# Performance work log

Hardware: AMD Instinct MI355X
Metric: run time of the kernel (lower is better)

## Reference

```python
import jax, jax.numpy as jnp
import numpy as np

N_QUBITS = 10
N_LAYERS = 4
BATCH = 16384
IN_FEAT = 256
HIDDEN = 128


def _ry(theta):
    # RY(theta) = [[cos(t/2), -sin(t/2)], [sin(t/2), cos(t/2)]]; theta: (B, n) -> (B, n, 2, 2)
    c = jnp.cos(theta / 2)
    s = jnp.sin(theta / 2)
    row0 = jnp.stack([c, -s], axis=-1)
    row1 = jnp.stack([s, c], axis=-1)
    return jnp.stack([row0, row1], axis=-2).astype(jnp.complex64)


def _rot(phi, theta, omega):
    # PennyLane Rot = RZ(omega) RY(theta) RZ(phi)
    c = jnp.cos(theta / 2)
    s = jnp.sin(theta / 2)
    ep = jnp.exp(-0.5j * (phi + omega))  # e^{-i(phi+omega)/2}
    em = jnp.exp(-0.5j * (phi - omega))  # e^{-i(phi-omega)/2}
    m00 = ep * c
    m01 = -jnp.conj(em) * s
    m10 = em * s
    m11 = jnp.conj(ep) * c
    return jnp.stack([jnp.stack([m00, m01]), jnp.stack([m10, m11])]).astype(jnp.complex64)


def _apply_1q(state, gate, w, n):
    # state: (B, 2**n); gate: (2,2) shared or (B,2,2) per-sample; wire w (wire 0 = MSB)
    B = state.shape[0]
    L, R = 2 ** w, 2 ** (n - w - 1)
    s = state.reshape(B, L, 2, R)
    if gate.ndim == 3:
        s = jnp.einsum('xab,xlbr->xlar', gate, s)
    else:
        s = jnp.einsum('ab,xlbr->xlar', gate, s)
    return s.reshape(B, -1)


def _cnot_perm(n, c, t):
    # CNOT is a basis permutation: flip target bit where control bit is 1 (static numpy)
    idx = np.arange(2 ** n)
    flip = idx ^ (1 << (n - 1 - t))
    ctrl = (idx >> (n - 1 - c)) & 1
    return np.where(ctrl == 1, flip, idx)


def _z_signs(n):
    # (n, 2**n) of +/-1: sign of PauliZ on each wire for each basis state
    idx = np.arange(2 ** n)
    bits = (idx[None, :] >> (n - 1 - np.arange(n)[:, None])) & 1
    return (1.0 - 2.0 * bits).astype(np.float32)


def _circuit(angles, qw):
    # angles: (B, n) embedding angles; qw: (L, n, 3) StronglyEntanglingLayers weights
    B, n = angles.shape
    L = qw.shape[0]
    state = jnp.zeros((B, 2 ** n), jnp.complex64).at[:, 0].set(1.0)
    ry = _ry(angles)  # (B, n, 2, 2) per-sample AngleEmbedding RY gates
    for w in range(n):
        state = _apply_1q(state, ry[:, w], w, n)
    for l in range(L):
        for w in range(n):
            state = _apply_1q(state, _rot(qw[l, w, 0], qw[l, w, 1], qw[l, w, 2]), w, n)
        r = (l % (n - 1)) + 1  # default StronglyEntanglingLayers ranges
        for i in range(n):
            state = state[:, _cnot_perm(n, i, (i + r) % n)]
    probs = jnp.abs(state) ** 2  # (B, 2**n)
    return probs @ jnp.asarray(_z_signs(n)).T  # (B, n) expval PauliZ per wire


def setup_inputs() -> dict:
    key = jax.random.key(0)
    ks = jax.random.split(key, 10)
    d = {
        'x': jax.random.normal(ks[0], (BATCH, IN_FEAT), jnp.float32),
        'W1': jax.random.normal(ks[1], (HIDDEN, IN_FEAT), jnp.float32) / np.sqrt(IN_FEAT),
        'b1': jnp.zeros((HIDDEN,), jnp.float32),
        'W2': jax.random.normal(ks[2], (N_QUBITS, HIDDEN), jnp.float32) / np.sqrt(HIDDEN),
        'b2': jnp.zeros((N_QUBITS,), jnp.float32),
        'q_weights': jax.random.normal(ks[3], (N_LAYERS, N_QUBITS, 3), jnp.float32) * 0.1,
        'W3': jax.random.normal(ks[4], (HIDDEN, N_QUBITS), jnp.float32) / np.sqrt(N_QUBITS),
        'b3': jnp.zeros((HIDDEN,), jnp.float32),
        'W4': jax.random.normal(ks[5], (1, HIDDEN), jnp.float32) / np.sqrt(HIDDEN),
        'b4': jnp.zeros((1,), jnp.float32),
    }
    return d


def reference(x, W1, b1, W2, b2, q_weights, W3, b3, W4, b4):
    # Encoder (dropout is identity in eval mode)
    h = jax.nn.relu(x @ W1.T + b1)
    angles = jnp.tanh(h @ W2.T + b2)  # (B, n_qubits)
    # Batched quantum state-vector simulation
    q = _circuit(angles, q_weights).astype(jnp.float32)  # (B, n_qubits)
    # Decoder
    d = jax.nn.relu(q @ W3.T + b3)
    return d @ W4.T + b4  # (B, 1)
```

## Files before the change

### kernel.cpp

```cpp
#include <hip/hip_runtime.h>
#include <math.h>

#define BATCH 16384
#define INFEAT 256
#define HID 128
#define NQ 10
#define NL 4
#define GSTRIDE 48

typedef float v2f __attribute__((ext_vector_type(2)));

template<int M>
__device__ __forceinline__ float lxor(float x) {
    if constexpr (M == 0) {
        return x;
    } else if constexpr (M < 4) {
        constexpr int ctrl = (0 ^ M) | ((1 ^ M) << 2) | ((2 ^ M) << 4) | ((3 ^ M) << 6);
        return __int_as_float(__builtin_amdgcn_update_dpp(
            __float_as_int(x), __float_as_int(x), ctrl, 0xF, 0xF, false));
    } else if constexpr (M == 8) {
        return __int_as_float(__builtin_amdgcn_update_dpp(
            __float_as_int(x), __float_as_int(x), 0x128, 0xF, 0xF, false));
    } else if constexpr (M < 32) {
        return __int_as_float(__builtin_amdgcn_ds_swizzle(
            __float_as_int(x), (M << 10) | 0x1F));
    } else {
        return __shfl_xor(x, M, 64);
    }
}

__device__ __forceinline__ float dpp_sum(float v) {
    v += __int_as_float(__builtin_amdgcn_update_dpp(0, __float_as_int(v), 0x111, 0xF, 0xF, true));
    v += __int_as_float(__builtin_amdgcn_update_dpp(0, __float_as_int(v), 0x112, 0xF, 0xF, true));
    v += __int_as_float(__builtin_amdgcn_update_dpp(0, __float_as_int(v), 0x114, 0xF, 0xF, true));
    v += __int_as_float(__builtin_amdgcn_update_dpp(0, __float_as_int(v), 0x118, 0xF, 0xF, true));
    v += __int_as_float(__builtin_amdgcn_update_dpp(0, __float_as_int(v), 0x142, 0xF, 0xF, true));
    v += __int_as_float(__builtin_amdgcn_update_dpp(0, __float_as_int(v), 0x143, 0xF, 0xF, true));
    return __int_as_float(__builtin_amdgcn_readlane(__float_as_int(v), 63));
}

template<int HALF>
__device__ __forceinline__ void swap_pl(float& a, float& b) {
    if constexpr (HALF == 32)
        asm("v_permlane32_swap_b32 %0, %1" : "+v"(a), "+v"(b));
    else
        asm("v_permlane16_swap_b32 %0, %1" : "+v"(a), "+v"(b));
}

__device__ __forceinline__ v2f pks_mul(v2f c, v2f a) {
    v2f d; asm("v_pk_mul_f32 %0, %1, %2" : "=v"(d) : "s"(c), "v"(a)); return d;
}
__device__ __forceinline__ v2f pks_fma(v2f c, v2f a, v2f b) {
    v2f d; asm("v_pk_fma_f32 %0, %1, %2, %3" : "=v"(d) : "s"(c), "v"(a), "v"(b)); return d;
}
__device__ __forceinline__ v2f pks_fma_swap(v2f c, v2f a, v2f b) {
    v2f d; asm("v_pk_fma_f32 %0, %1, %2, %3 op_sel:[0,1,0] op_sel_hi:[1,0,1]"
               : "=v"(d) : "s"(c), "v"(a), "v"(b)); return d;
}
__device__ __forceinline__ v2f pkv_mul_c(v2f c, v2f a) {
    v2f d; asm("v_pk_mul_f32 %0, %1, %2 op_sel:[0,0] op_sel_hi:[0,1]"
               : "=v"(d) : "v"(c), "v"(a)); return d;
}
__device__ __forceinline__ v2f pkv_fma_c(v2f c, v2f a, v2f b) {
    v2f d; asm("v_pk_fma_f32 %0, %1, %2, %3 op_sel:[0,0,0] op_sel_hi:[0,1,1]"
               : "=v"(d) : "v"(c), "v"(a), "v"(b)); return d;
}

__device__ __forceinline__ float getv(const v2f (&A)[8], int e) {
    return (e & 1) ? A[e >> 1].y : A[e >> 1].x;
}
__device__ __forceinline__ void setv(v2f (&A)[8], int e, float v) {
    if (e & 1) A[e >> 1].y = v; else A[e >> 1].x = v;
}


template<int KM>
__device__ __forceinline__ void reg_ry(const float* __restrict__ g,
                                       v2f (&AR)[8], v2f (&AI)[8]) {
    const v2f* __restrict__ gp = (const v2f*)g;
    const v2f C = gp[6], S = gp[7], Sn = gp[8];
#pragma unroll
    for (int k0 = 0; k0 < 8; ++k0) {
        if (k0 & KM) continue;
        const int k1 = k0 | KM;
        v2f A0 = AR[k0], A1 = AR[k1], I0 = AI[k0], I1 = AI[k1];
        AR[k0] = pks_fma(Sn, A1, pks_mul(C, A0));
        AI[k0] = pks_fma(Sn, I1, pks_mul(C, I0));
        AR[k1] = pks_fma(C, A1, pks_mul(S, A0));
        AI[k1] = pks_fma(C, I1, pks_mul(S, I0));
    }
}

__device__ __forceinline__ void q3_ry(const float* __restrict__ g,
                                      v2f (&AR)[8], v2f (&AI)[8]) {
    const v2f* __restrict__ gp = (const v2f*)g;
    const v2f C = gp[9], Ssw = gp[10];
#pragma unroll
    for (int k = 0; k < 8; ++k) {
        AR[k] = pks_fma_swap(Ssw, AR[k], pks_mul(C, AR[k]));
        AI[k] = pks_fma_swap(Ssw, AI[k], pks_mul(C, AI[k]));
    }
}

template<int HALF>
__device__ __forceinline__ void pl_ry(const float* __restrict__ g,
                                      v2f (&AR)[8], v2f (&AI)[8]) {
    const v2f* __restrict__ gp = (const v2f*)g;
    const v2f C = gp[6], S = gp[7], Sn = gp[8];
#pragma unroll
    for (int k0 = 0; k0 < 8; k0 += 2) {
        const int k1 = k0 + 1;
        float Xr0 = AR[k0].x, Xr1 = AR[k0].y, Yr0 = AR[k1].x, Yr1 = AR[k1].y;
        float Xi0 = AI[k0].x, Xi1 = AI[k0].y, Yi0 = AI[k1].x, Yi1 = AI[k1].y;
        swap_pl<HALF>(Xr0, Yr0); swap_pl<HALF>(Xr1, Yr1);
        swap_pl<HALF>(Xi0, Yi0); swap_pl<HALF>(Xi1, Yi1);
        v2f Xr; Xr.x = Xr0; Xr.y = Xr1;  v2f Yr; Yr.x = Yr0; Yr.y = Yr1;
        v2f Xi; Xi.x = Xi0; Xi.y = Xi1;  v2f Yi; Yi.x = Yi0; Yi.y = Yi1;
        v2f Pr = pks_fma(Sn, Yr, pks_mul(C, Xr));
        v2f Pi = pks_fma(Sn, Yi, pks_mul(C, Xi));
        v2f Qr = pks_fma(C, Yr, pks_mul(S, Xr));
        v2f Qi = pks_fma(C, Yi, pks_mul(S, Xi));
        float pr0 = Pr.x, pr1 = Pr.y, qr0 = Qr.x, qr1 = Qr.y;
        float pi0 = Pi.x, pi1 = Pi.y, qi0 = Qi.x, qi1 = Qi.y;
        swap_pl<HALF>(pr0, qr0); swap_pl<HALF>(pr1, qr1);
        swap_pl<HALF>(pi0, qi0); swap_pl<HALF>(pi1, qi1);
        AR[k0].x = pr0; AR[k0].y = pr1; AR[k1].x = qr0; AR[k1].y = qr1;
        AI[k0].x = pi0; AI[k0].y = pi1; AI[k1].x = qi0; AI[k1].y = qi1;
    }
}

template<int LB>
__device__ __forceinline__ void lane_ry(const float* __restrict__ g, int lane,
                                        v2f (&AR)[8], v2f (&AI)[8]) {
    const bool side = (lane >> LB) & 1;
    v2f Cm, Cp;
    Cm.x = g[8];
    Cp.x = side ? g[10] : g[9];
#pragma unroll
    for (int k = 0; k < 8; ++k) {
        v2f PR, PI;
        PR.x = lxor<(1 << LB)>(AR[k].x); PR.y = lxor<(1 << LB)>(AR[k].y);
        PI.x = lxor<(1 << LB)>(AI[k].x); PI.y = lxor<(1 << LB)>(AI[k].y);
        AR[k] = pkv_fma_c(Cp, PR, pkv_mul_c(Cm, AR[k]));
        AI[k] = pkv_fma_c(Cp, PI, pkv_mul_c(Cm, AI[k]));
    }
}

__device__ __forceinline__ void apply_diag(const float* __restrict__ dt, int lane,
                                           v2f (&AR)[8], v2f (&AI)[8]) {
    const float4* __restrict__ d4 = (const float4*)dt;
#pragma unroll
    for (int k = 0; k < 8; ++k) {
        float4 q = d4[k * 64 + lane];
        v2f CR; CR.x = q.x; CR.y = q.y;
        v2f CI; CI.x = q.z; CI.y = q.w;
        v2f ar = AR[k], ai = AI[k];
        v2f nR = __builtin_elementwise_fma(CI, -ai, CR * ar);
        v2f nI = __builtin_elementwise_fma(CI, ar, CR * ai);
        AR[k] = nR; AI[k] = nI;
    }
}

constexpr int rr_src(int rs, int e) {
    int s = e;
    for (int i = 3 - rs; i >= 0; --i) s ^= ((s >> (3 - i)) & 1) << (3 - i - rs);
    return s;
}
constexpr int rl_mask(int rs, int e) {
    int m = 0;
    for (int i = (4 - rs < 0 ? 0 : 4 - rs); i <= 3; ++i)
        if ((e >> (3 - i)) & 1) m |= 1 << (9 - i - rs);
    return m;
}

template<int L>
__device__ __forceinline__ void do_gates_ry(const float* __restrict__ gt, int lane,
                                            v2f (&AR)[8], v2f (&AI)[8]) {
    const float* __restrict__ gb = gt + L * NQ * GSTRIDE;
    reg_ry<4>(gb + 0 * GSTRIDE, AR, AI);
    reg_ry<2>(gb + 1 * GSTRIDE, AR, AI);
    reg_ry<1>(gb + 2 * GSTRIDE, AR, AI);
    q3_ry(gb + 3 * GSTRIDE, AR, AI);
    pl_ry<32>(gb + 4 * GSTRIDE, AR, AI);
    pl_ry<16>(gb + 5 * GSTRIDE, AR, AI);
    lane_ry<3>(gb + 6 * GSTRIDE, lane, AR, AI);
    lane_ry<2>(gb + 7 * GSTRIDE, lane, AR, AI);
    lane_ry<1>(gb + 8 * GSTRIDE, lane, AR, AI);
    lane_ry<0>(gb + 9 * GSTRIDE, lane, AR, AI);
}

template<int L>
__device__ __forceinline__ void do_move(int lane, v2f (&AR)[8], v2f (&AI)[8]) {
    constexpr int rs = L + 1;
    int y = lane;
#pragma unroll
    for (int i = 9 - rs; i >= 4; --i)
        y ^= ((y >> (9 - i)) & 1) << (9 - i - rs);
    const int base = y << 2;
    {
        float nr[16], ni[16];
#pragma unroll
        for (int e = 0; e < 16; ++e) {
            const int src = rr_src(rs, e);
            const int am  = rl_mask(rs, e) << 2;
            nr[e] = __int_as_float(__builtin_amdgcn_ds_bpermute(base ^ am, __float_as_int(getv(AR, src))));
            ni[e] = __int_as_float(__builtin_amdgcn_ds_bpermute(base ^ am, __float_as_int(getv(AI, src))));
        }
#pragma unroll
        for (int k = 0; k < 8; ++k) {
            AR[k].x = nr[2 * k]; AR[k].y = nr[2 * k + 1];
            AI[k].x = ni[2 * k]; AI[k].y = ni[2 * k + 1];
        }
    }
#pragma unroll
    for (int i = 10 - rs; i <= 9; ++i) {
        const bool p = (lane >> (9 - i)) & 1;
        const int tm = 1 << (13 - i - rs);
#pragma unroll
        for (int e = 0; e < 16; ++e) {
            if (!(e & tm)) {
                const int e1 = e | tm;
                float v0r = getv(AR, e), v1r = getv(AR, e1);
                setv(AR, e, p ? v1r : v0r); setv(AR, e1, p ? v0r : v1r);
                float v0i = getv(AI, e), v1i = getv(AI, e1);
                setv(AI, e, p ? v1i : v0i); setv(AI, e1, p ? v0i : v1i);
            }
        }
    }
}

__device__ __forceinline__ float ftanh(float s) {
    float e = __expf(2.f * s);
    return 1.f - 2.f / (e + 1.f);
}

__global__ void prep_kernel(const float* __restrict__ qw, const float* __restrict__ W1,
                            float* __restrict__ gtab, float* __restrict__ w1q,
                            float* __restrict__ dtab) {
    int tid = blockIdx.x * 256 + threadIdx.x;
    if (tid < 128 * 64) {
        int k2 = tid >> 6, l = tid & 63;
        float4 q;
        q.x = W1[(size_t)(2 * l)     * INFEAT + 2 * k2];
        q.y = W1[(size_t)(2 * l + 1) * INFEAT + 2 * k2];
        q.z = W1[(size_t)(2 * l)     * INFEAT + 2 * k2 + 1];
        q.w = W1[(size_t)(2 * l + 1) * INFEAT + 2 * k2 + 1];
        ((float4*)w1q)[tid] = q;
    }
    if (blockIdx.x == 0 && threadIdx.x < NL * NQ) {
        int t = threadIdx.x;
        float phi = qw[t * 3 + 0], th = qw[t * 3 + 1], om = qw[t * 3 + 2];
        float c = __cosf(th * 0.5f), s = __sinf(th * 0.5f);
        float a = 0.5f * (phi + om), b = 0.5f * (phi - om);
        float ca = __cosf(a), sa = __sinf(a);
        float cb = __cosf(b), sb = __sinf(b);
        float m00r = ca * c,  m00i = -sa * c;
        float m01r = -cb * s, m01i = -sb * s;
        float m10r = cb * s,  m10i = -sb * s;
        float m11r = ca * c,  m11i = sa * c;
        float* g = gtab + t * GSTRIDE;
        g[0] = m00r; g[1] = m00i; g[2] = m01r; g[3] = m01i;
        g[4] = m10r; g[5] = m10i; g[6] = m11r; g[7] = m11i;
        g[8] = c;  g[9] = -s;  g[10] = s;  g[11] = 0.f;
        g[12] = c;  g[13] = c;
        g[14] = s;  g[15] = s;
        g[16] = -s; g[17] = -s;
        g[18] = c;  g[19] = c;
        g[20] = -s; g[21] = s;
    }
    if (tid < 3 * 8 * 64) {
        const int ld = tid >> 9;
        const int k = (tid >> 6) & 7;
        const int lane = tid & 63;
        float cr[2], ci[2];
#pragma unroll
        for (int h = 0; h < 2; ++h) {
            const int n = ((2 * k + h) << 6) | lane;
            double a = 0.0;
            for (int w = 0; w < NQ; ++w) {
                const double bit = (double)((n >> (9 - w)) & 1) - 0.5;
                a += (double)qw[(ld + 1) * NQ * 3 + w * 3 + 0] * bit;
            }
            if (ld >= 1) {
                const int r = ld + 1;
                int m = n;
                for (int i = 9; i >= 0; --i) {
                    const int tq = (i + r) % 10;
                    m ^= ((m >> (9 - i)) & 1) << (9 - tq);
                }
                for (int w = 0; w < NQ; ++w) {
                    const double bit = (double)((m >> (9 - w)) & 1) - 0.5;
                    a += (double)qw[ld * NQ * 3 + w * 3 + 2] * bit;
                }
            }
            cr[h] = (float)cos(a);
            ci[h] = (float)sin(a);
        }
        float4 o;
        o.x = cr[0]; o.y = cr[1]; o.z = ci[0]; o.w = ci[1];
        ((float4*)dtab)[tid] = o;
    }
}

__global__ __launch_bounds__(256, 4) void fused_kernel(
    const float* __restrict__ x, const float* __restrict__ w1q,
    const float* __restrict__ b1, const float* __restrict__ W2,
    const float* __restrict__ b2, const float* __restrict__ gtab,
    const float* __restrict__ dtab,
    const float* __restrict__ W3, const float* __restrict__ b3,
    const float* __restrict__ W4, const float* __restrict__ b4,
    float* __restrict__ out)
{
    __shared__ float w3s[HID * 11];
    __shared__ float b3s[HID], w4s[HID];
    __shared__ float b4s;
    __shared__ v2f hpart[4][4][64];

    const int t = threadIdx.x;
    for (int f = t; f < HID * NQ; f += 256) {
        int c = f / NQ, k = f - c * NQ;
        w3s[c * 11 + k] = W3[f];
    }
    if (t < HID) { b3s[t] = b3[t]; w4s[t] = W4[t]; }
    if (t == 0) b4s = b4[0];

    const int lane = t & 63;
    const int wid = t >> 6;
    const int row0 = blockIdx.x * 4;
    const int ukw = __builtin_amdgcn_readfirstlane(wid);

    v2f acc[4];
#pragma unroll
    for (int r = 0; r < 4; ++r) acc[r] = (v2f)(0.f);
    const float4* __restrict__ xr0 = (const float4*)(x + (size_t)(row0 + 0) * INFEAT + ukw * 64);
    const float4* __restrict__ xr1 = (const float4*)(x + (size_t)(row0 + 1) * INFEAT + ukw * 64);
    const float4* __restrict__ xr2 = (const float4*)(x + (size_t)(row0 + 2) * INFEAT + ukw * 64);
    const float4* __restrict__ xr3 = (const float4*)(x + (size_t)(row0 + 3) * INFEAT + ukw * 64);
    const float4* __restrict__ w1p = (const float4*)w1q + (size_t)ukw * 32 * 64 + lane;
#pragma unroll 4
    for (int kk4 = 0; kk4 < 16; ++kk4) {
        float4 x0 = xr0[kk4], x1 = xr1[kk4], x2 = xr2[kk4], x3 = xr3[kk4];
        float xk[4][4] = {{x0.x, x0.y, x0.z, x0.w}, {x1.x, x1.y, x1.z, x1.w},
                          {x2.x, x2.y, x2.z, x2.w}, {x3.x, x3.y, x3.z, x3.w}};
        float4 q0 = w1p[(2 * kk4 + 0) * 64];
        float4 q1 = w1p[(2 * kk4 + 1) * 64];
        v2f w0; w0.x = q0.x; w0.y = q0.y;
        v2f w1; w1.x = q0.z; w1.y = q0.w;
        v2f w2; w2.x = q1.x; w2.y = q1.y;
        v2f w3; w3.x = q1.z; w3.y = q1.w;
#pragma unroll
        for (int r = 0; r < 4; ++r) {
            v2f xb;
            xb.x = xk[r][0]; xb.y = xk[r][0];
            acc[r] = __builtin_elementwise_fma(xb, w0, acc[r]);
            xb.x = xk[r][1]; xb.y = xk[r][1];
            acc[r] = __builtin_elementwise_fma(xb, w1, acc[r]);
            xb.x = xk[r][2]; xb.y = xk[r][2];
            acc[r] = __builtin_elementwise_fma(xb, w2, acc[r]);
            xb.x = xk[r][3]; xb.y = xk[r][3];
            acc[r] = __builtin_elementwise_fma(xb, w3, acc[r]);
        }
    }
#pragma unroll
    for (int r = 0; r < 4; ++r) hpart[wid][r][lane] = acc[r];
    __syncthreads();

    v2f hs = hpart[0][wid][lane];
    hs += hpart[1][wid][lane];
    hs += hpart[2][wid][lane];
    hs += hpart[3][wid][lane];
    float2 b1v = ((const float2*)b1)[lane];
    float h0 = fmaxf(hs.x + b1v.x, 0.f);
    float h1 = fmaxf(hs.y + b1v.y, 0.f);

    const int row = row0 + wid;

    float cth[NQ], sth[NQ];
#pragma unroll
    for (int w = 0; w < NQ; ++w) {
        float2 w2v = ((const float2*)(W2 + (size_t)w * HID))[lane];
        float aw = dpp_sum(fmaf(h0, w2v.x, h1 * w2v.y)) + b2[w];
        float th = ftanh(aw) * 0.5f;
        cth[w] = __cosf(th); sth[w] = __sinf(th);
    }

    float Lr, Li;
    {
        const float* __restrict__ g = gtab + 4 * GSTRIDE;
        bool bw = (lane >> 5) & 1;
        float g0 = bw ? g[4] : g[0], g1 = bw ? g[5] : g[1];
        float g2 = bw ? g[6] : g[2], g3 = bw ? g[7] : g[3];
        Lr = fmaf(g0, cth[4], g2 * sth[4]);
        Li = fmaf(g1, cth[4], g3 * sth[4]);
    }
#pragma unroll
    for (int w = 5; w < 10; ++w) {
        const float* __restrict__ g = gtab + w * GSTRIDE;
        bool bw = (lane >> (9 - w)) & 1;
        float g0 = bw ? g[4] : g[0], g1 = bw ? g[5] : g[1];
        float g2 = bw ? g[6] : g[2], g3 = bw ? g[7] : g[3];
        float fr = fmaf(g0, cth[w], g2 * sth[w]);
        float fi = fmaf(g1, cth[w], g3 * sth[w]);
        float nr = Lr * fr - Li * fi;
        float ni = Lr * fi + Li * fr;
        Lr = nr; Li = ni;
    }
    float q01r[4], q01i[4], q23r[4], q23i[4];
    {
        const float* __restrict__ ga = gtab + 0 * GSTRIDE;
        const float* __restrict__ gb = gtab + 1 * GSTRIDE;
        float a0r = fmaf(ga[0], cth[0], ga[2] * sth[0]);
        float a0i = fmaf(ga[1], cth[0], ga[3] * sth[0]);
        float b0r = fmaf(ga[4], cth[0], ga[6] * sth[0]);
        float b0i = fmaf(ga[5], cth[0], ga[7] * sth[0]);
        float a1r = fmaf(gb[0], cth[1], gb[2] * sth[1]);
        float a1i = fmaf(gb[1], cth[1], gb[3] * sth[1]);
        float b1r = fmaf(gb[4], cth[1], gb[6] * sth[1]);
        float b1i = fmaf(gb[5], cth[1], gb[7] * sth[1]);
#pragma unroll
        for (int j = 0; j < 4; ++j) {
            float f0r = (j & 2) ? b0r : a0r, f0i = (j & 2) ? b0i : a0i;
            float f1r = (j & 1) ? b1r : a1r, f1i = (j & 1) ? b1i : a1i;
            q01r[j] = f0r * f1r - f0i * f1i;
            q01i[j] = f0r * f1i + f0i * f1r;
        }
    }
    {
        const float* __restrict__ ga = gtab + 2 * GSTRIDE;
        const float* __restrict__ gb = gtab + 3 * GSTRIDE;
        float a2r = fmaf(ga[0], cth[2], ga[2] * sth[2]);
        float a2i = fmaf(ga[1], cth[2], ga[3] * sth[2]);
        float b2r = fmaf(ga[4], cth[2], ga[6] * sth[2]);
        float b2i = fmaf(ga[5], cth[2], ga[7] * sth[2]);
        float a3r = fmaf(gb[0], cth[3], gb[2] * sth[3]);
        float a3i = fmaf(gb[1], cth[3], gb[3] * sth[3]);
        float b3r = fmaf(gb[4], cth[3], gb[6] * sth[3]);
        float b3i = fmaf(gb[5], cth[3], gb[7] * sth[3]);
#pragma unroll
        for (int j = 0; j < 4; ++j) {
            float f2r = (j & 2) ? b2r : a2r, f2i = (j & 2) ? b2i : a2i;
            float f3r = (j & 1) ? b3r : a3r, f3i = (j & 1) ? b3i : a3i;
            q23r[j] = f2r * f3r - f2i * f3i;
            q23i[j] = f2r * f3i + f2i * f3r;
        }
    }
    v2f AR[8], AI[8];
#pragma unroll
    for (int e = 0; e < 16; ++e) {
        const int jh = e >> 2, jl = e & 3;
        float tr = q01r[jh] * q23r[jl] - q01i[jh] * q23i[jl];
        float ti = q01r[jh] * q23i[jl] + q01i[jh] * q23r[jl];
        float ar = tr * Lr - ti * Li;
        float ai = tr * Li + ti * Lr;
        setv(AR, e, ar); setv(AI, e, ai);
    }

    do_move<0>(lane, AR, AI);
    apply_diag(dtab + 0 * 2048, lane, AR, AI);
    do_gates_ry<1>(gtab, lane, AR, AI);
    do_move<1>(lane, AR, AI);
    apply_diag(dtab + 1 * 2048, lane, AR, AI);
    do_gates_ry<2>(gtab, lane, AR, AI);
    do_move<2>(lane, AR, AI);
    apply_diag(dtab + 2 * 2048, lane, AR, AI);
    do_gates_ry<3>(gtab, lane, AR, AI);
    do_move<3>(lane, AR, AI);

    v2f Pk[8];
#pragma unroll
    for (int k = 0; k < 8; ++k) Pk[k] = AR[k] * AR[k] + AI[k] * AI[k];
    v2f S = Pk[0] + Pk[1] + Pk[2] + Pk[3] + Pk[4] + Pk[5] + Pk[6] + Pk[7];
    float ptot = S.x + S.y;
    v2f Sq0 = Pk[4] + Pk[5] + Pk[6] + Pk[7];
    v2f Sq1 = Pk[2] + Pk[3] + Pk[6] + Pk[7];
    v2f Sq2 = Pk[1] + Pk[3] + Pk[5] + Pk[7];
    float es0 = dpp_sum(ptot - 2.f * (Sq0.x + Sq0.y));
    float es1 = dpp_sum(ptot - 2.f * (Sq1.x + Sq1.y));
    float es2 = dpp_sum(ptot - 2.f * (Sq2.x + Sq2.y));
    float es3 = dpp_sum(ptot - 2.f * S.y);
    float Wv = ptot;
    {
        float p;
        p = lxor<1>(Wv);  Wv = (lane & 1)  ? p - Wv : Wv + p;
        p = lxor<2>(Wv);  Wv = (lane & 2)  ? p - Wv : Wv + p;
        p = lxor<4>(Wv);  Wv = (lane & 4)  ? p - Wv : Wv + p;
        p = lxor<8>(Wv);  Wv = (lane & 8)  ? p - Wv : Wv + p;
        p = lxor<16>(Wv); Wv = (lane & 16) ? p - Wv : Wv + p;
        p = lxor<32>(Wv); Wv = (lane & 32) ? p - Wv : Wv + p;
    }
    const int wvi = __float_as_int(Wv);
    float es[NQ];
    es[0] = es0; es[1] = es1; es[2] = es2; es[3] = es3;
    es[4] = __int_as_float(__builtin_amdgcn_readlane(wvi, 32));
    es[5] = __int_as_float(__builtin_amdgcn_readlane(wvi, 16));
    es[6] = __int_as_float(__builtin_amdgcn_readlane(wvi, 8));
    es[7] = __int_as_float(__builtin_amdgcn_readlane(wvi, 4));
    es[8] = __int_as_float(__builtin_amdgcn_readlane(wvi, 2));
    es[9] = __int_as_float(__builtin_amdgcn_readlane(wvi, 1));

    float accv = 0.f;
#pragma unroll
    for (int j = 0; j < 2; ++j) {
        int c = lane + 64 * j;
        float d = b3s[c];
#pragma unroll
        for (int k = 0; k < NQ; ++k) d = fmaf(w3s[c * 11 + k], es[k], d);
        d = fmaxf(d, 0.f);
        accv = fmaf(d, w4s[c], accv);
    }
    accv = dpp_sum(accv);
    if (lane == 0) out[row] = accv + b4s;
}

extern "C" void kernel_launch(void* const* d_in, const int* in_sizes, int n_in,
                              void* d_out, int out_size, void* d_ws, size_t ws_size,
                              hipStream_t stream) {
    const float* x  = (const float*)d_in[0];
    const float* W1 = (const float*)d_in[1];
    const float* b1 = (const float*)d_in[2];
    const float* W2 = (const float*)d_in[3];
    const float* b2 = (const float*)d_in[4];
    const float* qw = (const float*)d_in[5];
    const float* W3 = (const float*)d_in[6];
    const float* b3 = (const float*)d_in[7];
    const float* W4 = (const float*)d_in[8];
    const float* b4 = (const float*)d_in[9];
    float* gtab = (float*)d_ws;
    float* w1q  = (float*)d_ws + 2048;
    float* dtab = (float*)d_ws + 2048 + 32768;
    float* out  = (float*)d_out;

    prep_kernel<<<(128 * 64 + 255) / 256, 256, 0, stream>>>(qw, W1, gtab, w1q, dtab);
    fused_kernel<<<BATCH / 4, 256, 0, stream>>>(x, w1q, b1, W2, b2, gtab, dtab, W3, b3, W4, b4, out);
}
```

Measured before the change: 187.2 us.

## Restructure fused kernel to one wave per block handling two rows

The fused kernel now launches 64-thread single-wave blocks that each process two batch rows. Each wave computes the full 256-wide first linear layer with packed FMAs that use op_sel to broadcast the x scalars, so the LDS partial-sum exchange and the block barrier are gone. It also drops the final CNOT permutation (do_move<3>) and instead folds it into sign-flipped Walsh-style expectation sums, and it reads W3/b3/W4 straight from global memory instead of staging them in shared memory. In exchange each wave reads its x rows and all of W1 serially over a longer loop, and W1 reuse per block drops from four rows to two.

```diff
diff --git a/kernel.cpp b/kernel.cpp
--- a/kernel.cpp
+++ b/kernel.cpp
@@ -57,6 +57,14 @@
     v2f d; asm("v_pk_fma_f32 %0, %1, %2, %3 op_sel:[0,1,0] op_sel_hi:[1,0,1]"
                : "=v"(d) : "s"(c), "v"(a), "v"(b)); return d;
 }
+__device__ __forceinline__ v2f pks_fma_clo(v2f c, v2f a, v2f b) {
+    v2f d; asm("v_pk_fma_f32 %0, %1, %2, %3 op_sel:[0,0,0] op_sel_hi:[0,1,1]"
+               : "=v"(d) : "s"(c), "v"(a), "v"(b)); return d;
+}
+__device__ __forceinline__ v2f pks_fma_chi(v2f c, v2f a, v2f b) {
+    v2f d; asm("v_pk_fma_f32 %0, %1, %2, %3 op_sel:[1,0,0] op_sel_hi:[1,1,1]"
+               : "=v"(d) : "s"(c), "v"(a), "v"(b)); return d;
+}
 __device__ __forceinline__ v2f pkv_mul_c(v2f c, v2f a) {
     v2f d; asm("v_pk_mul_f32 %0, %1, %2 op_sel:[0,0] op_sel_hi:[0,1]"
                : "=v"(d) : "v"(c), "v"(a)); return d;
@@ -72,7 +80,6 @@
 __device__ __forceinline__ void setv(v2f (&A)[8], int e, float v) {
     if (e & 1) A[e >> 1].y = v; else A[e >> 1].x = v;
 }
-
 
 template<int KM>
 __device__ __forceinline__ void reg_ry(const float* __restrict__ g,
@@ -302,7 +309,7 @@
     }
 }
 
-__global__ __launch_bounds__(256, 4) void fused_kernel(
+__global__ __launch_bounds__(64, 8) void fused_kernel(
     const float* __restrict__ x, const float* __restrict__ w1q,
     const float* __restrict__ b1, const float* __restrict__ W2,
     const float* __restrict__ b2, const float* __restrict__ gtab,
@@ -311,205 +318,193 @@
     const float* __restrict__ W4, const float* __restrict__ b4,
     float* __restrict__ out)
 {
-    __shared__ float w3s[HID * 11];
-    __shared__ float b3s[HID], w4s[HID];
-    __shared__ float b4s;
-    __shared__ v2f hpart[4][4][64];
-
-    const int t = threadIdx.x;
-    for (int f = t; f < HID * NQ; f += 256) {
-        int c = f / NQ, k = f - c * NQ;
-        w3s[c * 11 + k] = W3[f];
-    }
-    if (t < HID) { b3s[t] = b3[t]; w4s[t] = W4[t]; }
-    if (t == 0) b4s = b4[0];
-
-    const int lane = t & 63;
-    const int wid = t >> 6;
-    const int row0 = blockIdx.x * 4;
-    const int ukw = __builtin_amdgcn_readfirstlane(wid);
-
-    v2f acc[4];
-#pragma unroll
-    for (int r = 0; r < 4; ++r) acc[r] = (v2f)(0.f);
-    const float4* __restrict__ xr0 = (const float4*)(x + (size_t)(row0 + 0) * INFEAT + ukw * 64);
-    const float4* __restrict__ xr1 = (const float4*)(x + (size_t)(row0 + 1) * INFEAT + ukw * 64);
-    const float4* __restrict__ xr2 = (const float4*)(x + (size_t)(row0 + 2) * INFEAT + ukw * 64);
-    const float4* __restrict__ xr3 = (const float4*)(x + (size_t)(row0 + 3) * INFEAT + ukw * 64);
-    const float4* __restrict__ w1p = (const float4*)w1q + (size_t)ukw * 32 * 64 + lane;
+    const int lane = threadIdx.x;
+    const int rowA = blockIdx.x * 2;
+
+    v2f accA = (v2f)(0.f), accB = (v2f)(0.f);
+    const float4* __restrict__ xrA = (const float4*)(x + (size_t)rowA * INFEAT);
+    const float4* __restrict__ xrB = (const float4*)(x + (size_t)(rowA + 1) * INFEAT);
+    const float4* __restrict__ w1p = (const float4*)w1q + lane;
 #pragma unroll 4
-    for (int kk4 = 0; kk4 < 16; ++kk4) {
-        float4 x0 = xr0[kk4], x1 = xr1[kk4], x2 = xr2[kk4], x3 = xr3[kk4];
-        float xk[4][4] = {{x0.x, x0.y, x0.z, x0.w}, {x1.x, x1.y, x1.z, x1.w},
-                          {x2.x, x2.y, x2.z, x2.w}, {x3.x, x3.y, x3.z, x3.w}};
-        float4 q0 = w1p[(2 * kk4 + 0) * 64];
-        float4 q1 = w1p[(2 * kk4 + 1) * 64];
-        v2f w0; w0.x = q0.x; w0.y = q0.y;
-        v2f w1; w1.x = q0.z; w1.y = q0.w;
-        v2f w2; w2.x = q1.x; w2.y = q1.y;
-        v2f w3; w3.x = q1.z; w3.y = q1.w;
-#pragma unroll
-        for (int r = 0; r < 4; ++r) {
-            v2f xb;
-            xb.x = xk[r][0]; xb.y = xk[r][0];
-            acc[r] = __builtin_elementwise_fma(xb, w0, acc[r]);
-            xb.x = xk[r][1]; xb.y = xk[r][1];
-            acc[r] = __builtin_elementwise_fma(xb, w1, acc[r]);
-            xb.x = xk[r][2]; xb.y = xk[r][2];
-            acc[r] = __builtin_elementwise_fma(xb, w2, acc[r]);
-            xb.x = xk[r][3]; xb.y = xk[r][3];
-            acc[r] = __builtin_elementwise_fma(xb, w3, acc[r]);
-        }
-    }
-#pragma unroll
-    for (int r = 0; r < 4; ++r) hpart[wid][r][lane] = acc[r];
-    __syncthreads();
-
-    v2f hs = hpart[0][wid][lane];
-    hs += hpart[1][wid][lane];
-    hs += hpart[2][wid][lane];
-    hs += hpart[3][wid][lane];
+    for (int k4 = 0; k4 < 64; ++k4) {
+        float4 xa = xrA[k4], xb = xrB[k4];
+        float4 q0 = w1p[(2 * k4 + 0) * 64];
+        float4 q1 = w1p[(2 * k4 + 1) * 64];
+        v2f w0;  w0.x  = q0.x; w0.y  = q0.y;
+        v2f w1v; w1v.x = q0.z; w1v.y = q0.w;
+        v2f w2v; w2v.x = q1.x; w2v.y = q1.y;
+        v2f w3v; w3v.x = q1.z; w3v.y = q1.w;
+        v2f xa01; xa01.x = xa.x; xa01.y = xa.y;
+        v2f xa23; xa23.x = xa.z; xa23.y = xa.w;
+        v2f xb01; xb01.x = xb.x; xb01.y = xb.y;
+        v2f xb23; xb23.x = xb.z; xb23.y = xb.w;
+        accA = pks_fma_clo(xa01, w0,  accA);
+        accA = pks_fma_chi(xa01, w1v, accA);
+        accA = pks_fma_clo(xa23, w2v, accA);
+        accA = pks_fma_chi(xa23, w3v, accA);
+        accB = pks_fma_clo(xb01, w0,  accB);
+        accB = pks_fma_chi(xb01, w1v, accB);
+        accB = pks_fma_clo(xb23, w2v, accB);
+        accB = pks_fma_chi(xb23, w3v, accB);
+    }
     float2 b1v = ((const float2*)b1)[lane];
-    float h0 = fmaxf(hs.x + b1v.x, 0.f);
-    float h1 = fmaxf(hs.y + b1v.y, 0.f);
-
-    const int row = row0 + wid;
-
-    float cth[NQ], sth[NQ];
-#pragma unroll
-    for (int w = 0; w < NQ; ++w) {
-        float2 w2v = ((const float2*)(W2 + (size_t)w * HID))[lane];
-        float aw = dpp_sum(fmaf(h0, w2v.x, h1 * w2v.y)) + b2[w];
-        float th = ftanh(aw) * 0.5f;
-        cth[w] = __cosf(th); sth[w] = __sinf(th);
-    }
-
-    float Lr, Li;
-    {
-        const float* __restrict__ g = gtab + 4 * GSTRIDE;
-        bool bw = (lane >> 5) & 1;
-        float g0 = bw ? g[4] : g[0], g1 = bw ? g[5] : g[1];
-        float g2 = bw ? g[6] : g[2], g3 = bw ? g[7] : g[3];
-        Lr = fmaf(g0, cth[4], g2 * sth[4]);
-        Li = fmaf(g1, cth[4], g3 * sth[4]);
-    }
-#pragma unroll
-    for (int w = 5; w < 10; ++w) {
-        const float* __restrict__ g = gtab + w * GSTRIDE;
-        bool bw = (lane >> (9 - w)) & 1;
-        float g0 = bw ? g[4] : g[0], g1 = bw ? g[5] : g[1];
-        float g2 = bw ? g[6] : g[2], g3 = bw ? g[7] : g[3];
-        float fr = fmaf(g0, cth[w], g2 * sth[w]);
-        float fi = fmaf(g1, cth[w], g3 * sth[w]);
-        float nr = Lr * fr - Li * fi;
-        float ni = Lr * fi + Li * fr;
-        Lr = nr; Li = ni;
-    }
-    float q01r[4], q01i[4], q23r[4], q23i[4];
-    {
-        const float* __restrict__ ga = gtab + 0 * GSTRIDE;
-        const float* __restrict__ gb = gtab + 1 * GSTRIDE;
-        float a0r = fmaf(ga[0], cth[0], ga[2] * sth[0]);
-        float a0i = fmaf(ga[1], cth[0], ga[3] * sth[0]);
-        float b0r = fmaf(ga[4], cth[0], ga[6] * sth[0]);
-        float b0i = fmaf(ga[5], cth[0], ga[7] * sth[0]);
-        float a1r = fmaf(gb[0], cth[1], gb[2] * sth[1]);
-        float a1i = fmaf(gb[1], cth[1], gb[3] * sth[1]);
-        float b1r = fmaf(gb[4], cth[1], gb[6] * sth[1]);
-        float b1i = fmaf(gb[5], cth[1], gb[7] * sth[1]);
-#pragma unroll
-        for (int j = 0; j < 4; ++j) {
-            float f0r = (j & 2) ? b0r : a0r, f0i = (j & 2) ? b0i : a0i;
-            float f1r = (j & 1) ? b1r : a1r, f1i = (j & 1) ? b1i : a1i;
-            q01r[j] = f0r * f1r - f0i * f1i;
-            q01i[j] = f0r * f1i + f0i * f1r;
-        }
-    }
-    {
-        const float* __restrict__ ga = gtab + 2 * GSTRIDE;
-        const float* __restrict__ gb = gtab + 3 * GSTRIDE;
-        float a2r = fmaf(ga[0], cth[2], ga[2] * sth[2]);
-        float a2i = fmaf(ga[1], cth[2], ga[3] * sth[2]);
-        float b2r = fmaf(ga[4], cth[2], ga[6] * sth[2]);
-        float b2i = fmaf(ga[5], cth[2], ga[7] * sth[2]);
-        float a3r = fmaf(gb[0], cth[3], gb[2] * sth[3]);
-        float a3i = fmaf(gb[1], cth[3], gb[3] * sth[3]);
-        float b3r = fmaf(gb[4], cth[3], gb[6] * sth[3]);
-        float b3i = fmaf(gb[5], cth[3], gb[7] * sth[3]);
-#pragma unroll
-        for (int j = 0; j < 4; ++j) {
-            float f2r = (j & 2) ? b2r : a2r, f2i = (j & 2) ? b2i : a2i;
-            float f3r = (j & 1) ? b3r : a3r, f3i = (j & 1) ? b3i : a3i;
-            q23r[j] = f2r * f3r - f2i * f3i;
-            q23i[j] = f2r * f3i + f2i * f3r;
-        }
-    }
-    v2f AR[8], AI[8];
-#pragma unroll
-    for (int e = 0; e < 16; ++e) {
-        const int jh = e >> 2, jl = e & 3;
-        float tr = q01r[jh] * q23r[jl] - q01i[jh] * q23i[jl];
-        float ti = q01r[jh] * q23i[jl] + q01i[jh] * q23r[jl];
-        float ar = tr * Lr - ti * Li;
-        float ai = tr * Li + ti * Lr;
-        setv(AR, e, ar); setv(AI, e, ai);
-    }
-
-    do_move<0>(lane, AR, AI);
-    apply_diag(dtab + 0 * 2048, lane, AR, AI);
-    do_gates_ry<1>(gtab, lane, AR, AI);
-    do_move<1>(lane, AR, AI);
-    apply_diag(dtab + 1 * 2048, lane, AR, AI);
-    do_gates_ry<2>(gtab, lane, AR, AI);
-    do_move<2>(lane, AR, AI);
-    apply_diag(dtab + 2 * 2048, lane, AR, AI);
-    do_gates_ry<3>(gtab, lane, AR, AI);
-    do_move<3>(lane, AR, AI);
-
-    v2f Pk[8];
-#pragma unroll
-    for (int k = 0; k < 8; ++k) Pk[k] = AR[k] * AR[k] + AI[k] * AI[k];
-    v2f S = Pk[0] + Pk[1] + Pk[2] + Pk[3] + Pk[4] + Pk[5] + Pk[6] + Pk[7];
-    float ptot = S.x + S.y;
-    v2f Sq0 = Pk[4] + Pk[5] + Pk[6] + Pk[7];
-    v2f Sq1 = Pk[2] + Pk[3] + Pk[6] + Pk[7];
-    v2f Sq2 = Pk[1] + Pk[3] + Pk[5] + Pk[7];
-    float es0 = dpp_sum(ptot - 2.f * (Sq0.x + Sq0.y));
-    float es1 = dpp_sum(ptot - 2.f * (Sq1.x + Sq1.y));
-    float es2 = dpp_sum(ptot - 2.f * (Sq2.x + Sq2.y));
-    float es3 = dpp_sum(ptot - 2.f * S.y);
-    float Wv = ptot;
-    {
-        float p;
-        p = lxor<1>(Wv);  Wv = (lane & 1)  ? p - Wv : Wv + p;
-        p = lxor<2>(Wv);  Wv = (lane & 2)  ? p - Wv : Wv + p;
-        p = lxor<4>(Wv);  Wv = (lane & 4)  ? p - Wv : Wv + p;
-        p = lxor<8>(Wv);  Wv = (lane & 8)  ? p - Wv : Wv + p;
-        p = lxor<16>(Wv); Wv = (lane & 16) ? p - Wv : Wv + p;
-        p = lxor<32>(Wv); Wv = (lane & 32) ? p - Wv : Wv + p;
-    }
-    const int wvi = __float_as_int(Wv);
-    float es[NQ];
-    es[0] = es0; es[1] = es1; es[2] = es2; es[3] = es3;
-    es[4] = __int_as_float(__builtin_amdgcn_readlane(wvi, 32));
-    es[5] = __int_as_float(__builtin_amdgcn_readlane(wvi, 16));
-    es[6] = __int_as_float(__builtin_amdgcn_readlane(wvi, 8));
-    es[7] = __int_as_float(__builtin_amdgcn_readlane(wvi, 4));
-    es[8] = __int_as_float(__builtin_amdgcn_readlane(wvi, 2));
-    es[9] = __int_as_float(__builtin_amdgcn_readlane(wvi, 1));
-
-    float accv = 0.f;
-#pragma unroll
-    for (int j = 0; j < 2; ++j) {
-        int c = lane + 64 * j;
-        float d = b3s[c];
-#pragma unroll
-        for (int k = 0; k < NQ; ++k) d = fmaf(w3s[c * 11 + k], es[k], d);
-        d = fmaxf(d, 0.f);
-        accv = fmaf(d, w4s[c], accv);
-    }
-    accv = dpp_sum(accv);
-    if (lane == 0) out[row] = accv + b4s;
+    const float hA0 = fmaxf(accA.x + b1v.x, 0.f);
+    const float hA1 = fmaxf(accA.y + b1v.y, 0.f);
+    const float hB0 = fmaxf(accB.x + b1v.x, 0.f);
+    const float hB1 = fmaxf(accB.y + b1v.y, 0.f);
+
+#pragma unroll 1
+    for (int rr = 0; rr < 2; ++rr) {
+        const float h0 = rr ? hB0 : hA0;
+        const float h1 = rr ? hB1 : hA1;
+
+        float cth[NQ], sth[NQ];
+#pragma unroll
+        for (int w = 0; w < NQ; ++w) {
+            float2 w2v = ((const float2*)(W2 + (size_t)w * HID))[lane];
+            float aw = dpp_sum(fmaf(h0, w2v.x, h1 * w2v.y)) + b2[w];
+            float th = ftanh(aw) * 0.5f;
+            cth[w] = __cosf(th); sth[w] = __sinf(th);
+        }
+
+        float Lr, Li;
+        {
+            const float* __restrict__ g = gtab + 4 * GSTRIDE;
+            bool bw = (lane >> 5) & 1;
+            float g0 = bw ? g[4] : g[0], g1 = bw ? g[5] : g[1];
+            float g2 = bw ? g[6] : g[2], g3 = bw ? g[7] : g[3];
+            Lr = fmaf(g0, cth[4], g2 * sth[4]);
+            Li = fmaf(g1, cth[4], g3 * sth[4]);
+        }
+#pragma unroll
+        for (int w = 5; w < 10; ++w) {
+            const float* __restrict__ g = gtab + w * GSTRIDE;
+            bool bw = (lane >> (9 - w)) & 1;
+            float g0 = bw ? g[4] : g[0], g1 = bw ? g[5] : g[1];
+            float g2 = bw ? g[6] : g[2], g3 = bw ? g[7] : g[3];
+            float fr = fmaf(g0, cth[w], g2 * sth[w]);
+            float fi = fmaf(g1, cth[w], g3 * sth[w]);
+            float nr = Lr * fr - Li * fi;
+            float ni = Lr * fi + Li * fr;
+            Lr = nr; Li = ni;
+        }
+        float q01r[4], q01i[4], q23r[4], q23i[4];
+        {
+            const float* __restrict__ ga = gtab + 0 * GSTRIDE;
+            const float* __restrict__ gb = gtab + 1 * GSTRIDE;
+            float a0r = fmaf(ga[0], cth[0], ga[2] * sth[0]);
+            float a0i = fmaf(ga[1], cth[0], ga[3] * sth[0]);
+            float b0r = fmaf(ga[4], cth[0], ga[6] * sth[0]);
+            float b0i = fmaf(ga[5], cth[0], ga[7] * sth[0]);
+            float a1r = fmaf(gb[0], cth[1], gb[2] * sth[1]);
+            float a1i = fmaf(gb[1], cth[1], gb[3] * sth[1]);
+            float b1r = fmaf(gb[4], cth[1], gb[6] * sth[1]);
+            float b1i = fmaf(gb[5], cth[1], gb[7] * sth[1]);
+#pragma unroll
+            for (int j = 0; j < 4; ++j) {
+                float f0r = (j & 2) ? b0r : a0r, f0i = (j & 2) ? b0i : a0i;
+                float f1r = (j & 1) ? b1r : a1r, f1i = (j & 1) ? b1i : a1i;
+                q01r[j] = f0r * f1r - f0i * f1i;
+                q01i[j] = f0r * f1i + f0i * f1r;
+            }
+        }
+        {
+            const float* __restrict__ ga = gtab + 2 * GSTRIDE;
+            const float* __restrict__ gb = gtab + 3 * GSTRIDE;
+            float a2r = fmaf(ga[0], cth[2], ga[2] * sth[2]);
+            float a2i = fmaf(ga[1], cth[2], ga[3] * sth[2]);
+            float b2r = fmaf(ga[4], cth[2], ga[6] * sth[2]);
+            float b2i = fmaf(ga[5], cth[2], ga[7] * sth[2]);
+            float a3r = fmaf(gb[0], cth[3], gb[2] * sth[3]);
+            float a3i = fmaf(gb[1], cth[3], gb[3] * sth[3]);
+            float b3r = fmaf(gb[4], cth[3], gb[6] * sth[3]);
+            float b3i = fmaf(gb[5], cth[3], gb[7] * sth[3]);
+#pragma unroll
+            for (int j = 0; j < 4; ++j) {
+                float f2r = (j & 2) ? b2r : a2r, f2i = (j & 2) ? b2i : a2i;
+                float f3r = (j & 1) ? b3r : a3r, f3i = (j & 1) ? b3i : a3i;
+                q23r[j] = f2r * f3r - f2i * f3i;
+                q23i[j] = f2r * f3i + f2i * f3r;
+            }
+        }
+        v2f AR[8], AI[8];
+#pragma unroll
+        for (int e = 0; e < 16; ++e) {
+            const int jh = e >> 2, jl = e & 3;
+            float tr = q01r[jh] * q23r[jl] - q01i[jh] * q23i[jl];
+            float ti = q01r[jh] * q23i[jl] + q01i[jh] * q23r[jl];
+            float ar = tr * Lr - ti * Li;
+            float ai = tr * Li + ti * Lr;
+            setv(AR, e, ar); setv(AI, e, ai);
+        }
+
+        do_move<0>(lane, AR, AI);
+        apply_diag(dtab + 0 * 2048, lane, AR, AI);
+        do_gates_ry<1>(gtab, lane, AR, AI);
+        do_move<1>(lane, AR, AI);
+        apply_diag(dtab + 1 * 2048, lane, AR, AI);
+        do_gates_ry<2>(gtab, lane, AR, AI);
+        do_move<2>(lane, AR, AI);
+        apply_diag(dtab + 2 * 2048, lane, AR, AI);
+        do_gates_ry<3>(gtab, lane, AR, AI);
+
+        v2f Pk[8];
+#pragma unroll
+        for (int k = 0; k < 8; ++k) Pk[k] = AR[k] * AR[k] + AI[k] * AI[k];
+        v2f A0 = Pk[0] + Pk[1], B0 = Pk[2] + Pk[3], C0 = Pk[4] + Pk[5], D0 = Pk[6] + Pk[7];
+        v2f a0 = Pk[0] - Pk[1], b0 = Pk[2] - Pk[3], c0 = Pk[4] - Pk[5], d0 = Pk[6] - Pk[7];
+        v2f AB = A0 + B0, CD = C0 + D0;
+        v2f S  = AB + CD;
+        v2f W8 = AB - CD;
+        v2f V  = (A0 - B0) + (C0 - D0);
+        v2f E2 = a0 + b0, F2 = c0 + d0;
+        v2f T2v = E2 + F2, U = E2 - F2;
+        float t8  = W8.x + W8.y;
+        float t4  = V.x + V.y;
+        float t5  = V.x - V.y;
+        float t2  = T2v.x + T2v.y;
+        float t10 = U.x + U.y;
+        float t1  = S.x - S.y;
+        const bool p4  = lane & 4;
+        const bool p8  = lane & 8;
+        const bool p16 = lane & 16;
+        const bool p32 = lane & 32;
+        const bool p34 = ((lane >> 5) ^ (lane >> 1)) & 1;
+        const bool p17 = ((lane >> 4) ^ lane) & 1;
+        float es[NQ];
+        es[0] = dpp_sum(p8  ? -t10 : t10);
+        es[1] = dpp_sum(p4  ? -t5  : t5);
+        es[2] = dpp_sum(p34 ? -t10 : t10);
+        es[3] = dpp_sum(p17 ? -t5  : t5);
+        es[4] = dpp_sum(p32 ? -t8  : t8);
+        es[5] = dpp_sum(p16 ? -t4  : t4);
+        es[6] = dpp_sum(p8  ? -t2  : t2);
+        es[7] = dpp_sum(p4  ? -t1  : t1);
+        es[8] = dpp_sum(p34 ? -t8  : t8);
+        es[9] = dpp_sum(p17 ? -t4  : t4);
+
+        const float4* __restrict__ w3r = (const float4*)(W3 + (size_t)lane * 2 * NQ);
+        float4 wA = w3r[0], wB = w3r[1], wC = w3r[2], wD = w3r[3], wE = w3r[4];
+        float2 b3v = ((const float2*)b3)[lane];
+        float dd0 = b3v.x;
+        dd0 = fmaf(wA.x, es[0], dd0); dd0 = fmaf(wA.y, es[1], dd0);
+        dd0 = fmaf(wA.z, es[2], dd0); dd0 = fmaf(wA.w, es[3], dd0);
+        dd0 = fmaf(wB.x, es[4], dd0); dd0 = fmaf(wB.y, es[5], dd0);
+        dd0 = fmaf(wB.z, es[6], dd0); dd0 = fmaf(wB.w, es[7], dd0);
+        dd0 = fmaf(wC.x, es[8], dd0); dd0 = fmaf(wC.y, es[9], dd0);
+        float dd1 = b3v.y;
+        dd1 = fmaf(wC.z, es[0], dd1); dd1 = fmaf(wC.w, es[1], dd1);
+        dd1 = fmaf(wD.x, es[2], dd1); dd1 = fmaf(wD.y, es[3], dd1);
+        dd1 = fmaf(wD.z, es[4], dd1); dd1 = fmaf(wD.w, es[5], dd1);
+        dd1 = fmaf(wE.x, es[6], dd1); dd1 = fmaf(wE.y, es[7], dd1);
+        dd1 = fmaf(wE.z, es[8], dd1); dd1 = fmaf(wE.w, es[9], dd1);
+        dd0 = fmaxf(dd0, 0.f);
+        dd1 = fmaxf(dd1, 0.f);
+        float2 w4v = ((const float2*)W4)[lane];
+        float accv = fmaf(dd0, w4v.x, dd1 * w4v.y);
+        accv = dpp_sum(accv);
+        if (lane == 0) out[rowA + rr] = accv + b4[0];
+    }
 }
 
 extern "C" void kernel_launch(void* const* d_in, const int* in_sizes, int n_in,
@@ -531,5 +526,5 @@
     float* out  = (float*)d_out;
 
     prep_kernel<<<(128 * 64 + 255) / 256, 256, 0, stream>>>(qw, W1, gtab, w1q, dtab);
-    fused_kernel<<<BATCH / 4, 256, 0, stream>>>(x, w1q, b1, W2, b2, gtab, dtab, W3, b3, W4, b4, out);
-}
+    fused_kernel<<<BATCH / 2, 64, 0, stream>>>(x, w1q, b1, W2, b2, gtab, dtab, W3, b3, W4, b4, out);
+}
```

Measured after the change: 395.1 us. +111.0%, slower.
